# Optimization experiments

Measured on AMD Instinct MI355X. Metric: run time of the kernel, lower is better.

Reference implementation:

```python
import jax, jax.numpy as jnp
import numpy as np

B, T, V, E, H, C = 64, 512, 32000, 256, 512, 4

def setup_inputs() -> dict:
    key = jax.random.key(0)
    ks = jax.random.split(key, 8)
    s = 1.0 / np.sqrt(H)  # torch LSTM default init scale
    return {
        "x": jax.random.randint(ks[0], (B, T), 0, V),
        "emb": jax.random.normal(ks[1], (V, E), jnp.float32) * 0.1,
        "W_ih": jax.random.uniform(ks[2], (4 * H, E), jnp.float32, -s, s),
        "W_hh": jax.random.uniform(ks[3], (4 * H, H), jnp.float32, -s, s),
        "b_ih": jax.random.uniform(ks[4], (4 * H,), jnp.float32, -s, s),
        "b_hh": jax.random.uniform(ks[5], (4 * H,), jnp.float32, -s, s),
        "W_fc": jax.random.uniform(ks[6], (C, H), jnp.float32, -s, s),
        "b_fc": jax.random.uniform(ks[7], (C,), jnp.float32, -s, s),
    }

def _lstm_last_hidden(e, W_ih, W_hh, b_ih, b_hh):
    # e: [B,T,E]. Precompute input-side gate preactivations for all steps.
    xg = jnp.einsum('bte,ge->tbg', e, W_ih) + (b_ih + b_hh)  # [T,B,4H]
    h0 = jnp.zeros((e.shape[0], H), e.dtype)
    c0 = jnp.zeros((e.shape[0], H), e.dtype)

    def step(carry, xt):
        h, c = carry
        g = xt + h @ W_hh.T                       # [B,4H]
        i, f, gg, o = jnp.split(g, 4, axis=-1)    # torch gate order: i,f,g,o
        i = jax.nn.sigmoid(i)
        f = jax.nn.sigmoid(f)
        gg = jnp.tanh(gg)
        o = jax.nn.sigmoid(o)
        c = f * c + i * gg
        h = o * jnp.tanh(c)
        return (h, c), None

    (hT, _), _ = jax.lax.scan(step, (h0, c0), xg)
    return hT  # last hidden == lstm_out[:, -1, :] for unidirectional LSTM

def reference(x, emb, W_ih, W_hh, b_ih, b_hh, W_fc, b_fc):
    e = emb[x]                                    # [B,T,E] embedding lookup
    hT = _lstm_last_hidden(e, W_ih, W_hh, b_ih, b_hh)
    return hT @ W_fc.T + b_fc                     # [B,C] logits
```

## Files before the change

kernel.cpp:

```cpp
#include <hip/hip_runtime.h>
#include <hip/hip_bf16.h>

#define B_  64
#define T_  512
#define E_  256
#define H_  512
#define G4_ 2048
#define C_  4

typedef __attribute__((ext_vector_type(4))) float  f32x4;
typedef __attribute__((ext_vector_type(8))) __bf16 bf16x8;
typedef __attribute__((ext_vector_type(8))) short  short8;
typedef __attribute__((ext_vector_type(4))) short  s16x4;

union V16 { f32x4 f; bf16x8 b; short8 s; };

__device__ __forceinline__ float sigmoid_(float x) { return 1.0f / (1.0f + __expf(-x)); }
__device__ __forceinline__ float tanh_(float x)    { return 1.0f - 2.0f / (__expf(2.0f * x) + 1.0f); }

__device__ __forceinline__ short f2bf(float f) {
  union { float f; unsigned u; } v; v.f = f;
  return (short)((v.u + 0x7FFFu + ((v.u >> 16) & 1u)) >> 16);
}

__device__ __forceinline__ void store_short_llc(void* p, unsigned v) {
  asm volatile("global_store_short %0, %1, off sc0 sc1" :: "v"(p), "v"(v) : "memory");
}
__device__ __forceinline__ void store_dword_llc(void* p, float v) {
  asm volatile("global_store_dword %0, %1, off sc0 sc1" :: "v"(p), "v"(v) : "memory");
}
__device__ __forceinline__ f32x4 ld_b128_llc(const void* p) {
  f32x4 v;
  asm volatile("global_load_dwordx4 %0, %1, off sc0 sc1\n\ts_waitcnt vmcnt(0)"
               : "=&v"(v) : "v"(p) : "memory");
  return v;
}

__global__ __launch_bounds__(256, 1) void wih_conv(const float* __restrict__ W,
                                                   short* __restrict__ out) {
  const int i = (blockIdx.x * 256 + threadIdx.x) * 4;
  f32x4 v = *(const f32x4*)(W + i);
  s16x4 s;
  s[0] = f2bf(v[0]); s[1] = f2bf(v[1]); s[2] = f2bf(v[2]); s[3] = f2bf(v[3]);
  *(s16x4*)(out + i) = s;
}

template<bool WBF16>
__global__ __launch_bounds__(256, 1) void xg_kernel(
    const int* __restrict__ x, const float* __restrict__ emb,
    const void* __restrict__ Wv,
    __hip_bfloat16* __restrict__ xg)
{
  const int t   = blockIdx.x;
  const int tid = threadIdx.x;
  __shared__ int s_idx[B_];
  __shared__ __hip_bfloat16 s_e[B_][E_ + 8];

  if (tid < B_) s_idx[tid] = x[tid * T_ + t];
  __syncthreads();
  {
    int b = tid >> 2, ch = tid & 3;
    const float* src = emb + (size_t)s_idx[b] * E_ + ch * 64;
    short* dst = (short*)&s_e[b][ch * 64];
#pragma unroll
    for (int i = 0; i < 16; i++) {
      f32x4 v = *(const f32x4*)(src + i * 4);
      s16x4 s;
      s[0] = f2bf(v[0]); s[1] = f2bf(v[1]); s[2] = f2bf(v[2]); s[3] = f2bf(v[3]);
      *(s16x4*)(dst + i * 4) = s;
    }
  }
  __syncthreads();

  const int wv   = tid >> 6;
  const int lane = tid & 63;
  const int ln15 = lane & 15, quad = lane >> 4;

  V16 breg[4][8];
#pragma unroll
  for (int nt = 0; nt < 4; nt++)
#pragma unroll
    for (int ks = 0; ks < 8; ks++)
      breg[nt][ks].f = *(const f32x4*)(&s_e[nt * 16 + ln15][quad * 8 + ks * 32]);

  const int gbase = wv * 512;
  const size_t base_t = (size_t)t * (G4_ * B_);
  for (int mt = 0; mt < 32; mt++) {
    const int grow = gbase + mt * 16 + ln15;
    V16 areg[8];
    if constexpr (WBF16) {
      const short* arow = (const short*)Wv + (size_t)grow * E_ + quad * 8;
#pragma unroll
      for (int ks = 0; ks < 8; ks++)
        areg[ks].f = *(const f32x4*)(arow + ks * 32);
    } else {
      const float* arow = (const float*)Wv + (size_t)grow * E_ + quad * 8;
#pragma unroll
      for (int ks = 0; ks < 8; ks++) {
        f32x4 lo = *(const f32x4*)(arow + ks * 32);
        f32x4 hi = *(const f32x4*)(arow + ks * 32 + 4);
        short8 s;
        s[0] = f2bf(lo[0]); s[1] = f2bf(lo[1]); s[2] = f2bf(lo[2]); s[3] = f2bf(lo[3]);
        s[4] = f2bf(hi[0]); s[5] = f2bf(hi[1]); s[6] = f2bf(hi[2]); s[7] = f2bf(hi[3]);
        areg[ks].s = s;
      }
    }

    f32x4 acc[4];
#pragma unroll
    for (int nt = 0; nt < 4; nt++) acc[nt] = (f32x4){0.f, 0.f, 0.f, 0.f};
#pragma unroll
    for (int ks = 0; ks < 8; ks++)
#pragma unroll
      for (int nt = 0; nt < 4; nt++)
        acc[nt] = __builtin_amdgcn_mfma_f32_16x16x32_bf16(areg[ks].b, breg[nt][ks].b, acc[nt], 0, 0, 0);

    const int dbase = mt * 16 + quad * 4;
#pragma unroll
    for (int nt = 0; nt < 4; nt++) {
      const int batch = nt * 16 + ln15;
      s16x4 sv;
#pragma unroll
      for (int r = 0; r < 4; r++) sv[r] = f2bf(acc[nt][r]);
      *(s16x4*)((short*)xg + base_t + ((size_t)wv << 15) + ((size_t)batch << 9) + dbase) = sv;
    }
  }
}

__global__ __launch_bounds__(512, 2) void lstm_kernel(
    const float* __restrict__ W_hh,
    const float* __restrict__ b_ih, const float* __restrict__ b_hh,
    const float* __restrict__ W_fc, const float* __restrict__ b_fc,
    const __hip_bfloat16* __restrict__ xg,
    unsigned int* flags, __hip_bfloat16* hbuf , float* hT,
    float* out)
{
  const int tid  = threadIdx.x;
  const int blk  = blockIdx.x;
  const int g    = blk & 7;
  const int pd   = blk >> 3;
  const int d0   = pd * 64;
  const int wv   = tid >> 6;
  const int lane = tid & 63;
  const int ln15 = lane & 15, quad = lane >> 4;

  __shared__ __hip_bfloat16 s_h[16][520];
  __shared__ float s_pre[4][8][68];

  const int gate  = wv >> 1;
  const int dhalf = (wv & 1) * 32;
  V16 areg[2][16];
#pragma unroll
  for (int tau = 0; tau < 2; tau++) {
    const int grow = gate * 512 + d0 + dhalf + tau * 16 + ln15;
    const float* ap = W_hh + (size_t)grow * H_ + quad * 8;
#pragma unroll
    for (int ks = 0; ks < 16; ks++) {
      f32x4 lo = *(const f32x4*)(ap + ks * 32);
      f32x4 hi = *(const f32x4*)(ap + ks * 32 + 4);
      short8 s;
      s[0] = f2bf(lo[0]); s[1] = f2bf(lo[1]); s[2] = f2bf(lo[2]); s[3] = f2bf(lo[3]);
      s[4] = f2bf(hi[0]); s[5] = f2bf(hi[1]); s[6] = f2bf(hi[2]); s[7] = f2bf(hi[3]);
      areg[tau][ks].s = s;
    }
  }

  const int nb = tid >> 6;
  const int nd = tid & 63;
  const int gb = g * 8 + nb;
  const int dg = d0 + nd;
  const float bias_i = b_ih[dg]        + b_hh[dg];
  const float bias_f = b_ih[512 + dg]  + b_hh[512 + dg];
  const float bias_g = b_ih[1024 + dg] + b_hh[1024 + dg];
  const float bias_o = b_ih[1536 + dg] + b_hh[1536 + dg];
  float c = 0.0f;
  const int myflag = g * 16 + pd;

  *(f32x4*)&s_h[8 + (tid >> 6)][(tid & 63) * 8] = (f32x4){0.f, 0.f, 0.f, 0.f};

  for (int t = 0; t < T_; t++) {
    const int cur = t & 1, nxt = cur ^ 1;

    const size_t xoff = (size_t)t * (G4_ * B_) + ((size_t)gb << 9) + dg;
    const __hip_bfloat16 xgi = xg[xoff];
    const __hip_bfloat16 xgf = xg[xoff + (1u << 15)];
    const __hip_bfloat16 xgg = xg[xoff + (2u << 15)];
    const __hip_bfloat16 xgo = xg[xoff + (3u << 15)];

    if (tid < 8) {
      const unsigned* fp = flags + g * 16 + tid;
      while (__hip_atomic_load(fp, __ATOMIC_RELAXED, __HIP_MEMORY_SCOPE_AGENT) < (unsigned)t) {}
    }
    __syncthreads();

    {
      const short* hbase = (const short*)hbuf + (size_t)cur * (B_ * H_) + (size_t)(g * 8) * H_;
      f32x4 va = ld_b128_llc(hbase + tid * 8);
      *(f32x4*)&s_h[tid >> 6][(tid & 63) * 8] = va;
    }
    __syncthreads();

    f32x4 acc0 = (f32x4){0.f, 0.f, 0.f, 0.f};
    f32x4 acc1 = (f32x4){0.f, 0.f, 0.f, 0.f};
#pragma unroll
    for (int ks = 0; ks < 16; ks++) {
      V16 b0;
      b0.f = *(const f32x4*)&s_h[ln15][quad * 8 + ks * 32];
      acc0 = __builtin_amdgcn_mfma_f32_16x16x32_bf16(areg[0][ks].b, b0.b, acc0, 0, 0, 0);
      acc1 = __builtin_amdgcn_mfma_f32_16x16x32_bf16(areg[1][ks].b, b0.b, acc1, 0, 0, 0);
    }

    if (ln15 < 8) {
      *(f32x4*)&s_pre[gate][ln15][dhalf + quad * 4]      = acc0;
      *(f32x4*)&s_pre[gate][ln15][dhalf + 16 + quad * 4] = acc1;
    }
    __syncthreads();

    {
      const float pi = s_pre[0][nb][nd] + bias_i + __bfloat162float(xgi);
      const float pf = s_pre[1][nb][nd] + bias_f + __bfloat162float(xgf);
      const float pg = s_pre[2][nb][nd] + bias_g + __bfloat162float(xgg);
      const float po = s_pre[3][nb][nd] + bias_o + __bfloat162float(xgo);
      const float i_ = sigmoid_(pi), f_ = sigmoid_(pf);
      const float g_ = tanh_(pg),    o_ = sigmoid_(po);
      c = f_ * c + i_ * g_;
      const float h = o_ * tanh_(c);
      if (t < T_ - 1) {
        store_short_llc((short*)hbuf + (size_t)nxt * (B_ * H_) + (size_t)gb * H_ + dg,
                        (unsigned)(unsigned short)f2bf(h));
      } else {
        store_dword_llc(hT + gb * H_ + dg, h);
      }
    }
    __syncthreads();

    if (tid == 0)
      __hip_atomic_store(&flags[myflag], (unsigned)(t + 1),
                         __ATOMIC_RELAXED, __HIP_MEMORY_SCOPE_AGENT);
  }

  if (blk == 0) {
    if (tid < 64)
      while (__hip_atomic_load(flags + (tid >> 3) * 16 + (tid & 7),
                               __ATOMIC_RELAXED, __HIP_MEMORY_SCOPE_AGENT) < (unsigned)T_) {}
    __builtin_amdgcn_fence(__ATOMIC_ACQUIRE, "agent");
    __syncthreads();
    for (int o = tid; o < B_ * C_; o += 512) {
      const int b = o >> 2, cl = o & 3;
      const f32x4* hr = (const f32x4*)(hT + b * H_);
      const f32x4* wr = (const f32x4*)(W_fc + cl * H_);
      float s = 0.f;
      for (int d4 = 0; d4 < H_ / 4; d4++) {
        const f32x4 hv = hr[d4];
        const f32x4 wv4 = wr[d4];
        s += hv[0] * wv4[0] + hv[1] * wv4[1] + hv[2] * wv4[2] + hv[3] * wv4[3];
      }
      s += b_fc[cl];
      out[o] = s;
    }
  }
}

extern "C" void kernel_launch(void* const* d_in, const int* in_sizes, int n_in,
                              void* d_out, int out_size, void* d_ws, size_t ws_size,
                              hipStream_t stream) {
  const int*   x    = (const int*)d_in[0];
  const float* emb  = (const float*)d_in[1];
  const float* W_ih = (const float*)d_in[2];
  const float* W_hh = (const float*)d_in[3];
  const float* b_ih = (const float*)d_in[4];
  const float* b_hh = (const float*)d_in[5];
  const float* W_fc = (const float*)d_in[6];
  const float* b_fc = (const float*)d_in[7];
  float* out = (float*)d_out;

  char* ws = (char*)d_ws;
  const size_t XG_OFF  = 524288;
  const size_t XG_END  = XG_OFF + (size_t)T_ * G4_ * B_ * 2;
  const size_t NEEDED2 = XG_END + (size_t)G4_ * E_ * 2;
  if (ws_size < XG_END) return;

  unsigned int*   flags = (unsigned int*)ws;
  __hip_bfloat16* hbuf  = (__hip_bfloat16*)(ws + 4096);
  float*          hT    = (float*)(ws + 135168);
  __hip_bfloat16* xg    = (__hip_bfloat16*)(ws + XG_OFF);
  short*          wih16 = (short*)(ws + XG_END);

  (void)hipMemsetAsync(ws, 0, 135168, stream);

  if (ws_size >= NEEDED2) {
    wih_conv<<<512, 256, 0, stream>>>(W_ih, wih16);
    xg_kernel<true><<<T_, 256, 0, stream>>>(x, emb, wih16, xg);
  } else {
    xg_kernel<false><<<T_, 256, 0, stream>>>(x, emb, W_ih, xg);
  }
  lstm_kernel<<<64, 512, 0, stream>>>(W_hh, b_ih, b_hh, W_fc, b_fc, xg,
                                      flags, hbuf, hT, out);
}
```

Baseline: 1.251 ms.

## Fuse input-projection and LSTM recurrence into one kernel with per-step ready flags

```diff
diff --git a/kernel.cpp b/kernel.cpp
--- a/kernel.cpp
+++ b/kernel.cpp
@@ -29,11 +29,26 @@
 __device__ __forceinline__ void store_dword_llc(void* p, float v) {
   asm volatile("global_store_dword %0, %1, off sc0 sc1" :: "v"(p), "v"(v) : "memory");
 }
+__device__ __forceinline__ void store_dwordx2_llc(void* p, s16x4 v) {
+  asm volatile("global_store_dwordx2 %0, %1, off sc0 sc1" :: "v"(p), "v"(v) : "memory");
+}
 __device__ __forceinline__ f32x4 ld_b128_llc(const void* p) {
   f32x4 v;
   asm volatile("global_load_dwordx4 %0, %1, off sc0 sc1\n\ts_waitcnt vmcnt(0)"
                : "=&v"(v) : "v"(p) : "memory");
   return v;
+}
+__device__ __forceinline__ void prefetch_xg_llc(const short* p,
+                                                unsigned* r0, unsigned* r1,
+                                                unsigned* r2, unsigned* r3) {
+  asm volatile(
+      "global_load_ushort %0, %4, off sc0 sc1\n\t"
+      "global_load_ushort %1, %5, off sc0 sc1\n\t"
+      "global_load_ushort %2, %6, off sc0 sc1\n\t"
+      "global_load_ushort %3, %7, off sc0 sc1"
+      : "=&v"(*r0), "=&v"(*r1), "=&v"(*r2), "=&v"(*r3)
+      : "v"(p), "v"(p + 32768), "v"(p + 65536), "v"(p + 98304)
+      : "memory");
 }
 
 __global__ __launch_bounds__(256, 1) void wih_conv(const float* __restrict__ W,
@@ -45,107 +60,108 @@
   *(s16x4*)(out + i) = s;
 }
 
+union SMem {
+  struct { int idx[B_]; short e[B_][E_ + 8]; } xg;
+  struct { short h[16][520]; float pre[4][8][68]; } lstm;
+};
+
 template<bool WBF16>
-__global__ __launch_bounds__(256, 1) void xg_kernel(
+__global__ __launch_bounds__(512, 2) void fused_kernel(
     const int* __restrict__ x, const float* __restrict__ emb,
     const void* __restrict__ Wv,
-    __hip_bfloat16* __restrict__ xg)
+    const float* __restrict__ W_hh,
+    const float* __restrict__ b_ih, const float* __restrict__ b_hh,
+    const float* __restrict__ W_fc, const float* __restrict__ b_fc,
+    unsigned int* ctl, __hip_bfloat16* hbuf , float* hT,
+    __hip_bfloat16* xgbuf, float* out)
 {
-  const int t   = blockIdx.x;
-  const int tid = threadIdx.x;
-  __shared__ int s_idx[B_];
-  __shared__ __hip_bfloat16 s_e[B_][E_ + 8];
-
-  if (tid < B_) s_idx[tid] = x[tid * T_ + t];
-  __syncthreads();
-  {
-    int b = tid >> 2, ch = tid & 3;
-    const float* src = emb + (size_t)s_idx[b] * E_ + ch * 64;
-    short* dst = (short*)&s_e[b][ch * 64];
-#pragma unroll
-    for (int i = 0; i < 16; i++) {
-      f32x4 v = *(const f32x4*)(src + i * 4);
-      s16x4 s;
-      s[0] = f2bf(v[0]); s[1] = f2bf(v[1]); s[2] = f2bf(v[2]); s[3] = f2bf(v[3]);
-      *(s16x4*)(dst + i * 4) = s;
-    }
-  }
-  __syncthreads();
-
+  __shared__ SMem sm;
+  const int tid  = threadIdx.x;
+  const int blk  = blockIdx.x;
   const int wv   = tid >> 6;
   const int lane = tid & 63;
   const int ln15 = lane & 15, quad = lane >> 4;
 
-  V16 breg[4][8];
-#pragma unroll
-  for (int nt = 0; nt < 4; nt++)
-#pragma unroll
-    for (int ks = 0; ks < 8; ks++)
-      breg[nt][ks].f = *(const f32x4*)(&s_e[nt * 16 + ln15][quad * 8 + ks * 32]);
-
-  const int gbase = wv * 512;
-  const size_t base_t = (size_t)t * (G4_ * B_);
-  for (int mt = 0; mt < 32; mt++) {
-    const int grow = gbase + mt * 16 + ln15;
-    V16 areg[8];
-    if constexpr (WBF16) {
-      const short* arow = (const short*)Wv + (size_t)grow * E_ + quad * 8;
+  if (blk >= 64) {
+    const int t = blk - 64;
+    if (tid < B_) sm.xg.idx[tid] = x[tid * T_ + t];
+    __syncthreads();
+    {
+      int b = tid >> 3, ch = tid & 7;
+      const float* src = emb + (size_t)sm.xg.idx[b] * E_ + ch * 32;
+      short* dst = &sm.xg.e[b][ch * 32];
+#pragma unroll
+      for (int i = 0; i < 8; i++) {
+        f32x4 v = *(const f32x4*)(src + i * 4);
+        s16x4 s;
+        s[0] = f2bf(v[0]); s[1] = f2bf(v[1]); s[2] = f2bf(v[2]); s[3] = f2bf(v[3]);
+        *(s16x4*)(dst + i * 4) = s;
+      }
+    }
+    __syncthreads();
+
+    V16 breg[4][8];
+#pragma unroll
+    for (int nt = 0; nt < 4; nt++)
 #pragma unroll
       for (int ks = 0; ks < 8; ks++)
-        areg[ks].f = *(const f32x4*)(arow + ks * 32);
-    } else {
-      const float* arow = (const float*)Wv + (size_t)grow * E_ + quad * 8;
-#pragma unroll
-      for (int ks = 0; ks < 8; ks++) {
-        f32x4 lo = *(const f32x4*)(arow + ks * 32);
-        f32x4 hi = *(const f32x4*)(arow + ks * 32 + 4);
-        short8 s;
-        s[0] = f2bf(lo[0]); s[1] = f2bf(lo[1]); s[2] = f2bf(lo[2]); s[3] = f2bf(lo[3]);
-        s[4] = f2bf(hi[0]); s[5] = f2bf(hi[1]); s[6] = f2bf(hi[2]); s[7] = f2bf(hi[3]);
-        areg[ks].s = s;
-      }
-    }
-
-    f32x4 acc[4];
-#pragma unroll
-    for (int nt = 0; nt < 4; nt++) acc[nt] = (f32x4){0.f, 0.f, 0.f, 0.f};
-#pragma unroll
-    for (int ks = 0; ks < 8; ks++)
-#pragma unroll
-      for (int nt = 0; nt < 4; nt++)
-        acc[nt] = __builtin_amdgcn_mfma_f32_16x16x32_bf16(areg[ks].b, breg[nt][ks].b, acc[nt], 0, 0, 0);
-
-    const int dbase = mt * 16 + quad * 4;
-#pragma unroll
-    for (int nt = 0; nt < 4; nt++) {
-      const int batch = nt * 16 + ln15;
-      s16x4 sv;
-#pragma unroll
-      for (int r = 0; r < 4; r++) sv[r] = f2bf(acc[nt][r]);
-      *(s16x4*)((short*)xg + base_t + ((size_t)wv << 15) + ((size_t)batch << 9) + dbase) = sv;
-    }
-  }
-}
-
-__global__ __launch_bounds__(512, 2) void lstm_kernel(
-    const float* __restrict__ W_hh,
-    const float* __restrict__ b_ih, const float* __restrict__ b_hh,
-    const float* __restrict__ W_fc, const float* __restrict__ b_fc,
-    const __hip_bfloat16* __restrict__ xg,
-    unsigned int* flags, __hip_bfloat16* hbuf , float* hT,
-    float* out)
-{
-  const int tid  = threadIdx.x;
-  const int blk  = blockIdx.x;
+        breg[nt][ks].f = *(const f32x4*)(&sm.xg.e[nt * 16 + ln15][quad * 8 + ks * 32]);
+
+    const int gw  = wv & 3;
+    const int mt0 = (wv >> 2) * 16;
+    const int gbase = gw * 512;
+    const size_t base_t = (size_t)t * (G4_ * B_);
+    for (int mt = mt0; mt < mt0 + 16; mt++) {
+      const int grow = gbase + mt * 16 + ln15;
+      V16 areg[8];
+      if constexpr (WBF16) {
+        const short* arow = (const short*)Wv + (size_t)grow * E_ + quad * 8;
+#pragma unroll
+        for (int ks = 0; ks < 8; ks++)
+          areg[ks].f = *(const f32x4*)(arow + ks * 32);
+      } else {
+        const float* arow = (const float*)Wv + (size_t)grow * E_ + quad * 8;
+#pragma unroll
+        for (int ks = 0; ks < 8; ks++) {
+          f32x4 lo = *(const f32x4*)(arow + ks * 32);
+          f32x4 hi = *(const f32x4*)(arow + ks * 32 + 4);
+          short8 s;
+          s[0] = f2bf(lo[0]); s[1] = f2bf(lo[1]); s[2] = f2bf(lo[2]); s[3] = f2bf(lo[3]);
+          s[4] = f2bf(hi[0]); s[5] = f2bf(hi[1]); s[6] = f2bf(hi[2]); s[7] = f2bf(hi[3]);
+          areg[ks].s = s;
+        }
+      }
+
+      f32x4 acc[4];
+#pragma unroll
+      for (int nt = 0; nt < 4; nt++) acc[nt] = (f32x4){0.f, 0.f, 0.f, 0.f};
+#pragma unroll
+      for (int ks = 0; ks < 8; ks++)
+#pragma unroll
+        for (int nt = 0; nt < 4; nt++)
+          acc[nt] = __builtin_amdgcn_mfma_f32_16x16x32_bf16(areg[ks].b, breg[nt][ks].b, acc[nt], 0, 0, 0);
+
+      const int dbase = mt * 16 + quad * 4;
+#pragma unroll
+      for (int nt = 0; nt < 4; nt++) {
+        const int batch = nt * 16 + ln15;
+        s16x4 sv;
+#pragma unroll
+        for (int r = 0; r < 4; r++) sv[r] = f2bf(acc[nt][r]);
+        store_dwordx2_llc((short*)xgbuf + base_t + ((size_t)gw << 15) +
+                          ((size_t)batch << 9) + dbase, sv);
+      }
+    }
+    asm volatile("s_waitcnt vmcnt(0)" ::: "memory");
+    __syncthreads();
+    if (tid == 0)
+      __hip_atomic_store(ctl + 256 + t, 1u, __ATOMIC_RELAXED, __HIP_MEMORY_SCOPE_AGENT);
+    return;
+  }
+
   const int g    = blk & 7;
   const int pd   = blk >> 3;
   const int d0   = pd * 64;
-  const int wv   = tid >> 6;
-  const int lane = tid & 63;
-  const int ln15 = lane & 15, quad = lane >> 4;
-
-  __shared__ __hip_bfloat16 s_h[16][520];
-  __shared__ float s_pre[4][8][68];
 
   const int gate  = wv >> 1;
   const int dhalf = (wv & 1) * 32;
@@ -175,28 +191,29 @@
   const float bias_o = b_ih[1536 + dg] + b_hh[1536 + dg];
   float c = 0.0f;
   const int myflag = g * 16 + pd;
-
-  *(f32x4*)&s_h[8 + (tid >> 6)][(tid & 63) * 8] = (f32x4){0.f, 0.f, 0.f, 0.f};
+  const short* xg_s = (const short*)xgbuf;
+
+  *(f32x4*)&sm.lstm.h[8 + (tid >> 6)][(tid & 63) * 8] = (f32x4){0.f, 0.f, 0.f, 0.f};
 
   for (int t = 0; t < T_; t++) {
     const int cur = t & 1, nxt = cur ^ 1;
 
-    const size_t xoff = (size_t)t * (G4_ * B_) + ((size_t)gb << 9) + dg;
-    const __hip_bfloat16 xgi = xg[xoff];
-    const __hip_bfloat16 xgf = xg[xoff + (1u << 15)];
-    const __hip_bfloat16 xgg = xg[xoff + (2u << 15)];
-    const __hip_bfloat16 xgo = xg[xoff + (3u << 15)];
-
     if (tid < 8) {
-      const unsigned* fp = flags + g * 16 + tid;
+      const unsigned* fp = ctl + g * 16 + tid;
       while (__hip_atomic_load(fp, __ATOMIC_RELAXED, __HIP_MEMORY_SCOPE_AGENT) < (unsigned)t) {}
-    }
-    __syncthreads();
+    } else if (tid == 8) {
+      while (__hip_atomic_load(ctl + 256 + t, __ATOMIC_RELAXED, __HIP_MEMORY_SCOPE_AGENT) == 0u) {}
+    }
+    __syncthreads();
+
+    unsigned px0, px1, px2, px3;
+    prefetch_xg_llc(xg_s + (size_t)t * (G4_ * B_) + ((size_t)gb << 9) + dg,
+                    &px0, &px1, &px2, &px3);
 
     {
       const short* hbase = (const short*)hbuf + (size_t)cur * (B_ * H_) + (size_t)(g * 8) * H_;
       f32x4 va = ld_b128_llc(hbase + tid * 8);
-      *(f32x4*)&s_h[tid >> 6][(tid & 63) * 8] = va;
+      *(f32x4*)&sm.lstm.h[tid >> 6][(tid & 63) * 8] = va;
     }
     __syncthreads();
 
@@ -205,22 +222,22 @@
 #pragma unroll
     for (int ks = 0; ks < 16; ks++) {
       V16 b0;
-      b0.f = *(const f32x4*)&s_h[ln15][quad * 8 + ks * 32];
+      b0.f = *(const f32x4*)&sm.lstm.h[ln15][quad * 8 + ks * 32];
       acc0 = __builtin_amdgcn_mfma_f32_16x16x32_bf16(areg[0][ks].b, b0.b, acc0, 0, 0, 0);
       acc1 = __builtin_amdgcn_mfma_f32_16x16x32_bf16(areg[1][ks].b, b0.b, acc1, 0, 0, 0);
     }
 
     if (ln15 < 8) {
-      *(f32x4*)&s_pre[gate][ln15][dhalf + quad * 4]      = acc0;
-      *(f32x4*)&s_pre[gate][ln15][dhalf + 16 + quad * 4] = acc1;
+      *(f32x4*)&sm.lstm.pre[gate][ln15][dhalf + quad * 4]      = acc0;
+      *(f32x4*)&sm.lstm.pre[gate][ln15][dhalf + 16 + quad * 4] = acc1;
     }
     __syncthreads();
 
     {
-      const float pi = s_pre[0][nb][nd] + bias_i + __bfloat162float(xgi);
-      const float pf = s_pre[1][nb][nd] + bias_f + __bfloat162float(xgf);
-      const float pg = s_pre[2][nb][nd] + bias_g + __bfloat162float(xgg);
-      const float po = s_pre[3][nb][nd] + bias_o + __bfloat162float(xgo);
+      const float pi = sm.lstm.pre[0][nb][nd] + bias_i + __uint_as_float(px0 << 16);
+      const float pf = sm.lstm.pre[1][nb][nd] + bias_f + __uint_as_float(px1 << 16);
+      const float pg = sm.lstm.pre[2][nb][nd] + bias_g + __uint_as_float(px2 << 16);
+      const float po = sm.lstm.pre[3][nb][nd] + bias_o + __uint_as_float(px3 << 16);
       const float i_ = sigmoid_(pi), f_ = sigmoid_(pf);
       const float g_ = tanh_(pg),    o_ = sigmoid_(po);
       c = f_ * c + i_ * g_;
@@ -235,13 +252,13 @@
     __syncthreads();
 
     if (tid == 0)
-      __hip_atomic_store(&flags[myflag], (unsigned)(t + 1),
+      __hip_atomic_store(ctl + myflag, (unsigned)(t + 1),
                          __ATOMIC_RELAXED, __HIP_MEMORY_SCOPE_AGENT);
   }
 
   if (blk == 0) {
     if (tid < 64)
-      while (__hip_atomic_load(flags + (tid >> 3) * 16 + (tid & 7),
+      while (__hip_atomic_load(ctl + (tid >> 3) * 16 + (tid & 7),
                                __ATOMIC_RELAXED, __HIP_MEMORY_SCOPE_AGENT) < (unsigned)T_) {}
     __builtin_amdgcn_fence(__ATOMIC_ACQUIRE, "agent");
     __syncthreads();
@@ -280,20 +297,20 @@
   const size_t NEEDED2 = XG_END + (size_t)G4_ * E_ * 2;
   if (ws_size < XG_END) return;
 
-  unsigned int*   flags = (unsigned int*)ws;
+  unsigned int*   ctl   = (unsigned int*)ws;
   __hip_bfloat16* hbuf  = (__hip_bfloat16*)(ws + 4096);
   float*          hT    = (float*)(ws + 135168);
-  __hip_bfloat16* xg    = (__hip_bfloat16*)(ws + XG_OFF);
+  __hip_bfloat16* xgbuf = (__hip_bfloat16*)(ws + XG_OFF);
   short*          wih16 = (short*)(ws + XG_END);
 
   (void)hipMemsetAsync(ws, 0, 135168, stream);
 
   if (ws_size >= NEEDED2) {
     wih_conv<<<512, 256, 0, stream>>>(W_ih, wih16);
-    xg_kernel<true><<<T_, 256, 0, stream>>>(x, emb, wih16, xg);
+    fused_kernel<true><<<576, 512, 0, stream>>>(
+        x, emb, wih16, W_hh, b_ih, b_hh, W_fc, b_fc, ctl, hbuf, hT, xgbuf, out);
   } else {
-    xg_kernel<false><<<T_, 256, 0, stream>>>(x, emb, W_ih, xg);
-  }
-  lstm_kernel<<<64, 512, 0, stream>>>(W_hh, b_ih, b_hh, W_fc, b_fc, xg,
-                                      flags, hbuf, hT, out);
-}
+    fused_kernel<false><<<576, 512, 0, stream>>>(
+        x, emb, W_ih, W_hh, b_ih, b_hh, W_fc, b_fc, ctl, hbuf, hT, xgbuf, out);
+  }
+}
```

New measurement: 1.954 ms. 56.2% more time.
